# Kernel tuning notes

Hardware: AMD Instinct MI355X
Metric: run time of the kernel (lower is better)

The kernel has to match this reference:

```python
import jax, jax.numpy as jnp
import numpy as np

B, C, H, W = 32, 256, 64, 64
CI = C // 2  # inter_channels


def conv1x1(x, w, b):
    # x: [B, Cin, H, W], w: [Cout, Cin], b: [Cout]
    return jnp.einsum('bchw,oc->bohw', x, w) + b[None, :, None, None]


def setup_inputs() -> dict:
    key = jax.random.key(0)
    ks = jax.random.split(key, 9)
    s_in = 1.0 / np.sqrt(C)
    s_ci = 1.0 / np.sqrt(CI)
    return {
        'x': jax.random.normal(ks[0], (B, C, H, W), dtype=jnp.float32),
        'theta_w': jax.random.normal(ks[1], (CI, C), dtype=jnp.float32) * s_in,
        'theta_b': jax.random.normal(ks[2], (CI,), dtype=jnp.float32) * s_in,
        'phi_w': jax.random.normal(ks[3], (CI, C), dtype=jnp.float32) * s_in,
        'phi_b': jax.random.normal(ks[4], (CI,), dtype=jnp.float32) * s_in,
        'g_w': jax.random.normal(ks[5], (CI, C), dtype=jnp.float32) * s_in,
        'g_b': jax.random.normal(ks[6], (CI,), dtype=jnp.float32) * s_in,
        'out_w': jax.random.normal(ks[7], (C, CI), dtype=jnp.float32) * s_ci,
        'out_b': jax.random.normal(ks[8], (C,), dtype=jnp.float32) * s_ci,
    }


def reference(x, theta_w, theta_b, phi_w, phi_b, g_w, g_b, out_w, out_b):
    b, c, h, w = x.shape
    n = h * w
    theta = conv1x1(x, theta_w, theta_b).reshape(b, CI, n)  # [B, Ci, N]
    phi = conv1x1(x, phi_w, phi_b).reshape(b, CI, n)        # [B, Ci, N]
    g = conv1x1(x, g_w, g_b).reshape(b, CI, n)              # [B, Ci, N]
    # f[b,i,j] = sum_n theta[b,i,n] * phi[b,j,n]  -> [B, Ci, Ci]
    f = jnp.einsum('bin,bjn->bij', theta, phi)
    f_div_c = jax.nn.softmax(f, axis=-1)
    # y[b,j,n] = sum_i f_div_c[b,i,j] * g[b,i,n]  (uses f^T, per the torch permute)
    y = jnp.einsum('bij,bin->bjn', f_div_c, g)  # [B, Ci, N]
    # Faithful to torch: permute(0,2,1).contiguous().view(B, Ci, H, W)
    # -> a memory reshape of the [B, N, Ci] layout, NOT a transpose.
    y = jnp.transpose(y, (0, 2, 1)).reshape(b, CI, h, w)
    y = conv1x1(y, out_w, out_b)  # [B, C, H, W]
    return x + y
```

## Files before the change

### kernel.cpp

```cpp
#include <hip/hip_runtime.h>

#define B_ 32
#define C_ 256
#define CI_ 128
#define N_ 4096

typedef unsigned int u32;
typedef unsigned short u16;
typedef __attribute__((ext_vector_type(8))) short s8v;
typedef __attribute__((ext_vector_type(4))) float f4v;

__device__ __forceinline__ u16 f2bs(float f) {
    union { float f; u32 u; } c; c.f = f;
    u32 u = c.u + 0x7FFFu + ((c.u >> 16) & 1u);
    return (u16)(u >> 16);
}
__device__ __forceinline__ float bs2f(u16 s) {
    union { u32 u; float f; } c; c.u = ((u32)s) << 16; return c.f;
}
__device__ __forceinline__ void split2(float x, u16& h, u16& l) {
    h = f2bs(x);
    l = f2bs(x - bs2f(h));
}

#define MFMA16(a, b, c) __builtin_amdgcn_mfma_f32_16x16x32_bf16((a), (b), (c), 0, 0, 0)

__global__ __launch_bounds__(64) void sx_kernel(
    const float* __restrict__ x, float* __restrict__ sx)
{
    const int t = blockIdx.x, b = blockIdx.y, lane = threadIdx.x;
    const float4* row = (const float4*)(x + ((size_t)(b * C_ + t)) * N_);
    float s = 0.f;
    for (int k = lane; k < N_ / 4; k += 64) {
        float4 v = row[k];
        s += v.x + v.y + v.z + v.w;
    }
    #pragma unroll
    for (int off = 32; off > 0; off >>= 1) s += __shfl_down(s, off);
    if (lane == 0) sx[b * C_ + t] = s;
}

__global__ __launch_bounds__(256) void gram_mfma(
    const float* __restrict__ x, float* __restrict__ outp)
{
    const int zb = blockIdx.z;
    const int b = zb >> 3, ks = zb & 7;
    const int i0 = blockIdx.y * 128, j0 = blockIdx.x * 128;
    const int tid = threadIdx.x;
    const int w = tid >> 6, l = tid & 63, lm = l & 15, lq = l >> 4;

    __shared__ u16 Ah[128 * 40], Al[128 * 40], Bh[128 * 40], Bl[128 * 40];

    f4v acc[2][8];
    #pragma unroll
    for (int mi = 0; mi < 2; ++mi)
        #pragma unroll
        for (int ni = 0; ni < 8; ++ni) acc[mi][ni] = (f4v){0.f, 0.f, 0.f, 0.f};

    const int srow = tid >> 3;
    const int sc4  = (tid & 7) * 4;

    const int kbeg = ks * 512, kend = kbeg + 512;
    for (int k0 = kbeg; k0 < kend; k0 += 32) {
        #pragma unroll
        for (int rr = 0; rr < 4; ++rr) {
            int row = rr * 32 + srow;
            float4 va = *(const float4*)(x + (((size_t)(b * C_ + i0 + row)) << 12) + k0 + sc4);
            float4 vb = *(const float4*)(x + (((size_t)(b * C_ + j0 + row)) << 12) + k0 + sc4);
            u16 h0, h1, h2, h3, l0, l1, l2, l3;
            split2(va.x, h0, l0); split2(va.y, h1, l1);
            split2(va.z, h2, l2); split2(va.w, h3, l3);
            *(uint2*)&Ah[row * 40 + sc4] = make_uint2((u32)h0 | ((u32)h1 << 16),
                                                      (u32)h2 | ((u32)h3 << 16));
            *(uint2*)&Al[row * 40 + sc4] = make_uint2((u32)l0 | ((u32)l1 << 16),
                                                      (u32)l2 | ((u32)l3 << 16));
            split2(vb.x, h0, l0); split2(vb.y, h1, l1);
            split2(vb.z, h2, l2); split2(vb.w, h3, l3);
            *(uint2*)&Bh[row * 40 + sc4] = make_uint2((u32)h0 | ((u32)h1 << 16),
                                                      (u32)h2 | ((u32)h3 << 16));
            *(uint2*)&Bl[row * 40 + sc4] = make_uint2((u32)l0 | ((u32)l1 << 16),
                                                      (u32)l2 | ((u32)l3 << 16));
        }
        __syncthreads();

        const int kofs = lq * 8;
        s8v ah[2], al2[2];
        #pragma unroll
        for (int mi = 0; mi < 2; ++mi) {
            int arow = w * 32 + mi * 16 + lm;
            ah[mi]  = *(const s8v*)&Ah[arow * 40 + kofs];
            al2[mi] = *(const s8v*)&Al[arow * 40 + kofs];
        }
        #pragma unroll
        for (int ni = 0; ni < 8; ++ni) {
            int brow = ni * 16 + lm;
            s8v bh = *(const s8v*)&Bh[brow * 40 + kofs];
            s8v bl = *(const s8v*)&Bl[brow * 40 + kofs];
            #pragma unroll
            for (int mi = 0; mi < 2; ++mi) {
                acc[mi][ni] = MFMA16(ah[mi],  bh, acc[mi][ni]);
                acc[mi][ni] = MFMA16(ah[mi],  bl, acc[mi][ni]);
                acc[mi][ni] = MFMA16(al2[mi], bh, acc[mi][ni]);
            }
        }
        __syncthreads();
    }
    float* Gp = outp + (((size_t)(b * 256 + 128)) << 12) + (size_t)ks * 65536;
    #pragma unroll
    for (int mi = 0; mi < 2; ++mi)
        #pragma unroll
        for (int ni = 0; ni < 8; ++ni)
            #pragma unroll
            for (int r = 0; r < 4; ++r) {
                int gi = i0 + w * 32 + mi * 16 + lq * 4 + r;
                int gj = j0 + ni * 16 + lm;
                Gp[(size_t)gi * 256 + gj] = acc[mi][ni][r];
            }
}

__global__ __launch_bounds__(256) void g_reduce(
    const float* __restrict__ outp, float* __restrict__ G)
{
    int f = blockIdx.x * 256 + threadIdx.x;
    int b = f >> 14;
    int r4 = (f & 16383) << 2;
    const float* src = outp + (((size_t)(b * 256 + 128)) << 12) + r4;
    float4 s = *(const float4*)(src);
    #pragma unroll
    for (int k = 1; k < 8; ++k) {
        float4 v = *(const float4*)(src + (size_t)k * 65536);
        s.x += v.x; s.y += v.y; s.z += v.z; s.w += v.w;
    }
    *(float4*)(G + ((size_t)b << 16) + r4) = s;
}

__global__ __launch_bounds__(512, 2) void mid_kernel(
    const float* __restrict__ G,
    const float* __restrict__ tw, const float* __restrict__ tb,
    const float* __restrict__ pw, const float* __restrict__ pb,
    const float* __restrict__ sx,
    const float* __restrict__ gw, const float* __restrict__ gb,
    u16* __restrict__ Mh, float* __restrict__ rj)
{
    const int b = blockIdx.x;
    const int tid = threadIdx.x;
    const int w = tid >> 6, l = tid & 63, lm = l & 15, lq = l >> 4;
    const int wr = w >> 2, wc = w & 3;

    __shared__ __attribute__((aligned(16))) char smem[157696];
    float* t12s = (float*)(smem + 155648);
    float* sxs  = (float*)(smem + 156672);
    u16* TwTh = (u16*)(smem);
    u16* TwTl = (u16*)(smem + 10240);
    u16* GTh  = (u16*)(smem + 20480);
    u16* GTl  = (u16*)(smem + 40960);
    u16* A1h = (u16*)(smem);
    u16* A1l = (u16*)(smem + 67584);
    u16* PwTh = (u16*)(smem + 135168);
    u16* PwTl = (u16*)(smem + 145408);
    float* Ff = (float*)(smem);
    u16* fsmTh = (u16*)(smem + 69632);
    u16* fsmTl = (u16*)(smem + 104448);
    u16* GwTh = (u16*)(smem);
    u16* GwTl = (u16*)(smem + 20480);

    if (tid < 256) sxs[tid] = sx[b * 256 + tid];
    __syncthreads();
    {
        const int oid = tid >> 1, half = tid & 1;
        const float* wrow = (oid < 128) ? (tw + oid * 256) : (pw + (oid - 128) * 256);
        float s = 0.f;
        for (int t = half * 128; t < half * 128 + 128; ++t) s += wrow[t] * sxs[t];
        s += __shfl_xor(s, 1);
        if (half == 0) t12s[oid] = s;
    }
    __syncthreads();

    f4v acc[4][4];
    #pragma unroll
    for (int mi = 0; mi < 4; ++mi)
        #pragma unroll
        for (int ni = 0; ni < 4; ++ni) acc[mi][ni] = (f4v){0.f, 0.f, 0.f, 0.f};

    for (int t0 = 0; t0 < C_; t0 += 32) {
        {
            int i = tid >> 2, tg = (tid & 3) * 8;
            float4 v0 = *(const float4*)(tw + i * 256 + t0 + tg);
            float4 v1 = *(const float4*)(tw + i * 256 + t0 + tg + 4);
            u16 h0,h1,h2,h3,l0,l1,l2,l3;
            split2(v0.x,h0,l0); split2(v0.y,h1,l1); split2(v0.z,h2,l2); split2(v0.w,h3,l3);
            *(uint2*)&TwTh[i*40+tg]   = make_uint2((u32)h0|((u32)h1<<16),(u32)h2|((u32)h3<<16));
            *(uint2*)&TwTl[i*40+tg]   = make_uint2((u32)l0|((u32)l1<<16),(u32)l2|((u32)l3<<16));
            split2(v1.x,h0,l0); split2(v1.y,h1,l1); split2(v1.z,h2,l2); split2(v1.w,h3,l3);
            *(uint2*)&TwTh[i*40+tg+4] = make_uint2((u32)h0|((u32)h1<<16),(u32)h2|((u32)h3<<16));
            *(uint2*)&TwTl[i*40+tg+4] = make_uint2((u32)l0|((u32)l1<<16),(u32)l2|((u32)l3<<16));
        }
        {
            int u = tid >> 1, tg = (tid & 1) * 16;
            const float* gp = G + ((size_t)b << 16) + (size_t)u * 256 + t0 + tg;
            #pragma unroll
            for (int q = 0; q < 4; ++q) {
                float4 v = *(const float4*)(gp + q * 4);
                u16 h0,h1,h2,h3,l0,l1,l2,l3;
                split2(v.x,h0,l0); split2(v.y,h1,l1); split2(v.z,h2,l2); split2(v.w,h3,l3);
                *(uint2*)&GTh[u*40+tg+q*4] = make_uint2((u32)h0|((u32)h1<<16),(u32)h2|((u32)h3<<16));
                *(uint2*)&GTl[u*40+tg+q*4] = make_uint2((u32)l0|((u32)l1<<16),(u32)l2|((u32)l3<<16));
            }
        }
        __syncthreads();
        const int kofs = lq * 8;
        s8v ah[4], al[4];
        #pragma unroll
        for (int mi = 0; mi < 4; ++mi) {
            int ai = wr * 64 + mi * 16 + lm;
            ah[mi] = *(const s8v*)&TwTh[ai * 40 + kofs];
            al[mi] = *(const s8v*)&TwTl[ai * 40 + kofs];
        }
        #pragma unroll
        for (int ni = 0; ni < 4; ++ni) {
            int bu = wc * 64 + ni * 16 + lm;
            s8v bh = *(const s8v*)&GTh[bu * 40 + kofs];
            s8v bl = *(const s8v*)&GTl[bu * 40 + kofs];
            #pragma unroll
            for (int mi = 0; mi < 4; ++mi) {
                acc[mi][ni] = MFMA16(ah[mi], bh, acc[mi][ni]);
                acc[mi][ni] = MFMA16(ah[mi], bl, acc[mi][ni]);
                acc[mi][ni] = MFMA16(al[mi], bh, acc[mi][ni]);
            }
        }
        __syncthreads();
    }
    #pragma unroll
    for (int mi = 0; mi < 4; ++mi)
        #pragma unroll
        for (int ni = 0; ni < 4; ++ni)
            #pragma unroll
            for (int r = 0; r < 4; ++r) {
                int i = wr * 64 + mi * 16 + lq * 4 + r;
                int u = wc * 64 + ni * 16 + lm;
                u16 h, lo; split2(acc[mi][ni][r], h, lo);
                A1h[i * 264 + u] = h; A1l[i * 264 + u] = lo;
            }
    __syncthreads();

    f4v acc2[4][2];
    #pragma unroll
    for (int mi = 0; mi < 4; ++mi)
        #pragma unroll
        for (int ni = 0; ni < 2; ++ni) acc2[mi][ni] = (f4v){0.f, 0.f, 0.f, 0.f};

    for (int u0 = 0; u0 < C_; u0 += 32) {
        {
            int j = tid >> 2, ug = (tid & 3) * 8;
            float4 v0 = *(const float4*)(pw + j * 256 + u0 + ug);
            float4 v1 = *(const float4*)(pw + j * 256 + u0 + ug + 4);
            u16 h0,h1,h2,h3,l0,l1,l2,l3;
            split2(v0.x,h0,l0); split2(v0.y,h1,l1); split2(v0.z,h2,l2); split2(v0.w,h3,l3);
            *(uint2*)&PwTh[j*40+ug]   = make_uint2((u32)h0|((u32)h1<<16),(u32)h2|((u32)h3<<16));
            *(uint2*)&PwTl[j*40+ug]   = make_uint2((u32)l0|((u32)l1<<16),(u32)l2|((u32)l3<<16));
            split2(v1.x,h0,l0); split2(v1.y,h1,l1); split2(v1.z,h2,l2); split2(v1.w,h3,l3);
            *(uint2*)&PwTh[j*40+ug+4] = make_uint2((u32)h0|((u32)h1<<16),(u32)h2|((u32)h3<<16));
            *(uint2*)&PwTl[j*40+ug+4] = make_uint2((u32)l0|((u32)l1<<16),(u32)l2|((u32)l3<<16));
        }
        __syncthreads();
        const int kofs = lq * 8;
        s8v ah[4], al[4];
        #pragma unroll
        for (int mi = 0; mi < 4; ++mi) {
            int ai = wr * 64 + mi * 16 + lm;
            ah[mi] = *(const s8v*)&A1h[ai * 264 + u0 + kofs];
            al[mi] = *(const s8v*)&A1l[ai * 264 + u0 + kofs];
        }
        #pragma unroll
        for (int ni = 0; ni < 2; ++ni) {
            int bj = wc * 32 + ni * 16 + lm;
            s8v bh = *(const s8v*)&PwTh[bj * 40 + kofs];
            s8v bl = *(const s8v*)&PwTl[bj * 40 + kofs];
            #pragma unroll
            for (int mi = 0; mi < 4; ++mi) {
                acc2[mi][ni] = MFMA16(ah[mi], bh, acc2[mi][ni]);
                acc2[mi][ni] = MFMA16(ah[mi], bl, acc2[mi][ni]);
                acc2[mi][ni] = MFMA16(al[mi], bh, acc2[mi][ni]);
            }
        }
        __syncthreads();
    }
    #pragma unroll
    for (int ni = 0; ni < 2; ++ni) {
        int j = wc * 32 + ni * 16 + lm;
        float pbv = pb[j], t2v = t12s[128 + j];
        #pragma unroll
        for (int mi = 0; mi < 4; ++mi)
            #pragma unroll
            for (int r = 0; r < 4; ++r) {
                int i = wr * 64 + mi * 16 + lq * 4 + r;
                float val = acc2[mi][ni][r] + t12s[i] * pbv
                          + tb[i] * (t2v + 4096.0f * pbv);
                Ff[i * 136 + j] = val;
            }
    }
    __syncthreads();

    {
        const int i = tid >> 2, sub = tid & 3;
        float vv[32];
        #pragma unroll
        for (int c = 0; c < 32; ++c) vv[c] = Ff[i * 136 + sub * 32 + c];
        float m = vv[0];
        #pragma unroll
        for (int c = 1; c < 32; ++c) m = fmaxf(m, vv[c]);
        m = fmaxf(m, __shfl_xor(m, 1));
        m = fmaxf(m, __shfl_xor(m, 2));
        float s = 0.f;
        #pragma unroll
        for (int c = 0; c < 32; ++c) { vv[c] = __expf(vv[c] - m); s += vv[c]; }
        s += __shfl_xor(s, 1);
        s += __shfl_xor(s, 2);
        float inv = 1.0f / s;
        #pragma unroll
        for (int c = 0; c < 32; ++c) {
            int j = sub * 32 + c;
            u16 h, lo; split2(vv[c] * inv, h, lo);
            fsmTh[j * 136 + i] = h; fsmTl[j * 136 + i] = lo;
        }
    }
    __syncthreads();

    if (tid < 128) {
        float s = 0.f;
        for (int i = 0; i < 128; ++i)
            s += (bs2f(fsmTh[tid * 136 + i]) + bs2f(fsmTl[tid * 136 + i])) * gb[i];
        rj[b * 128 + tid] = s;
    }

    f4v acc3[4][4];
    #pragma unroll
    for (int mi = 0; mi < 4; ++mi)
        #pragma unroll
        for (int ni = 0; ni < 4; ++ni) acc3[mi][ni] = (f4v){0.f, 0.f, 0.f, 0.f};

    for (int i0 = 0; i0 < CI_; i0 += 32) {
        {
            int ir = tid >> 4, tg = (tid & 15) * 16;
            const float* gp = gw + (size_t)(i0 + ir) * 256 + tg;
            float vv[16];
            *(float4*)&vv[0]  = *(const float4*)(gp + 0);
            *(float4*)&vv[4]  = *(const float4*)(gp + 4);
            *(float4*)&vv[8]  = *(const float4*)(gp + 8);
            *(float4*)&vv[12] = *(const float4*)(gp + 12);
            const int chb = ir >> 3, il = ir & 7;
            #pragma unroll
            for (int jj = 0; jj < 16; ++jj) {
                int t = tg + jj;
                int ch = chb ^ ((t >> 4) & 3);
                u16 h, lo; split2(vv[jj], h, lo);
                GwTh[t * 40 + ch * 8 + il] = h;
                GwTl[t * 40 + ch * 8 + il] = lo;
            }
        }
        __syncthreads();
        s8v ah[4], al[4];
        #pragma unroll
        for (int mi = 0; mi < 4; ++mi) {
            int aj = wr * 64 + mi * 16 + lm;
            ah[mi] = *(const s8v*)&fsmTh[aj * 136 + i0 + lq * 8];
            al[mi] = *(const s8v*)&fsmTl[aj * 136 + i0 + lq * 8];
        }
        #pragma unroll
        for (int ni = 0; ni < 4; ++ni) {
            int bt = wc * 64 + ni * 16 + lm;
            int co = (lq ^ ((bt >> 4) & 3)) << 3;
            s8v bh = *(const s8v*)&GwTh[bt * 40 + co];
            s8v bl = *(const s8v*)&GwTl[bt * 40 + co];
            #pragma unroll
            for (int mi = 0; mi < 4; ++mi) {
                acc3[mi][ni] = MFMA16(ah[mi], bh, acc3[mi][ni]);
                acc3[mi][ni] = MFMA16(ah[mi], bl, acc3[mi][ni]);
                acc3[mi][ni] = MFMA16(al[mi], bh, acc3[mi][ni]);
            }
        }
        __syncthreads();
    }
    #pragma unroll
    for (int mi = 0; mi < 4; ++mi)
        #pragma unroll
        for (int ni = 0; ni < 4; ++ni)
            #pragma unroll
            for (int r = 0; r < 4; ++r) {
                int j = wr * 64 + mi * 16 + lq * 4 + r;
                int t = wc * 64 + ni * 16 + lm;
                Mh[(size_t)b * 32768 + (size_t)j * 256 + t] = f2bs(acc3[mi][ni][r]);
            }
}

__global__ __launch_bounds__(256) void owh_kernel(
    const float* __restrict__ ow, u16* __restrict__ Owh)
{
    int i = (blockIdx.x * 256 + threadIdx.x) * 4;
    float4 v = *(const float4*)(ow + i);
    u16 a = f2bs(v.x), b = f2bs(v.y), c = f2bs(v.z), d = f2bs(v.w);
    *(uint2*)&Owh[i] = make_uint2((u32)a | ((u32)b << 16), (u32)c | ((u32)d << 16));
}

__global__ __launch_bounds__(256) void y_kernel(
    const u16* __restrict__ Mh, const float* __restrict__ rj,
    const float* __restrict__ x, float* __restrict__ outp)
{
    const int nb = blockIdx.x, b = blockIdx.y;
    const int n0 = nb * 128;
    const int tid = threadIdx.x;
    const int w = tid >> 6, l = tid & 63, lm = l & 15, lq = l >> 4;

    __shared__ u16 Bs[128 * 40];

    f4v acc[2][8];
    #pragma unroll
    for (int mi = 0; mi < 2; ++mi)
        #pragma unroll
        for (int ni = 0; ni < 8; ++ni) acc[mi][ni] = (f4v){0.f, 0.f, 0.f, 0.f};

    const int tt = tid >> 3;
    const int nn0 = (tid & 7) * 16;

    for (int t0 = 0; t0 < C_; t0 += 32) {
        const float* xr = x + (((size_t)(b * C_ + t0 + tt)) << 12) + n0 + nn0;
        float vv[16];
        *(float4*)&vv[0]  = *(const float4*)(xr + 0);
        *(float4*)&vv[4]  = *(const float4*)(xr + 4);
        *(float4*)&vv[8]  = *(const float4*)(xr + 8);
        *(float4*)&vv[12] = *(const float4*)(xr + 12);
        const int chb = tt >> 3, tl = tt & 7;
        #pragma unroll
        for (int j = 0; j < 16; ++j) {
            int row = nn0 + j;
            int ch = chb ^ ((row >> 4) & 3);
            Bs[row * 40 + ch * 8 + tl] = f2bs(vv[j]);
        }
        __syncthreads();

        s8v af[2];
        #pragma unroll
        for (int mi = 0; mi < 2; ++mi)
            af[mi] = *(const s8v*)(Mh + (size_t)b * 32768
                     + (size_t)(w * 32 + mi * 16 + lm) * 256 + t0 + lq * 8);
        #pragma unroll
        for (int ni = 0; ni < 8; ++ni) {
            int row = ni * 16 + lm;
            s8v bf = *(const s8v*)&Bs[row * 40 + ((lq ^ ((row >> 4) & 3)) << 3)];
            acc[0][ni] = MFMA16(af[0], bf, acc[0][ni]);
            acc[1][ni] = MFMA16(af[1], bf, acc[1][ni]);
        }
        __syncthreads();
    }
    #pragma unroll
    for (int mi = 0; mi < 2; ++mi) {
        const int s0 = w * 32 + mi * 16 + lq * 4;
        float rjv[4];
        #pragma unroll
        for (int r = 0; r < 4; ++r) rjv[r] = rj[b * 128 + s0 + r];
        #pragma unroll
        for (int ni = 0; ni < 8; ++ni) {
            int nn = ni * 16 + lm;
            int z = (n0 + nn) >> 5;
            int q = nn & 31;
            float4 st;
            st.x = acc[mi][ni][0] + rjv[0];
            st.y = acc[mi][ni][1] + rjv[1];
            st.z = acc[mi][ni][2] + rjv[2];
            st.w = acc[mi][ni][3] + rjv[3];
            *(float4*)(outp + (((size_t)(b * C_ + z)) << 12) + 128 * q + s0) = st;
        }
    }
}

__global__ __launch_bounds__(256) void out_kernel(
    float* outp, const u16* __restrict__ Owh, const float* __restrict__ ob,
    const float* __restrict__ x)
{
    const int pt = blockIdx.x, b = blockIdx.y;
    const int p0 = pt * 64;
    const int tid = threadIdx.x;
    const int w = tid >> 6, l = tid & 63, lm = l & 15, lq = l >> 4;

    __shared__ __attribute__((aligned(16))) u16 Zs[64 * 136];
    float* Fsc = (float*)Zs;

    const int zz = tid >> 2;
    const int pp0 = (tid & 3) * 16;
    #pragma unroll
    for (int zb = 0; zb < 128; zb += 64) {
        const int zc = zb + zz;
        const float* yr = outp + (((size_t)(b * C_ + zc)) << 12) + p0 + pp0;
        float vv[16];
        *(float4*)&vv[0]  = *(const float4*)(yr + 0);
        *(float4*)&vv[4]  = *(const float4*)(yr + 4);
        *(float4*)&vv[8]  = *(const float4*)(yr + 8);
        *(float4*)&vv[12] = *(const float4*)(yr + 12);
        const int chb = zc >> 3, zl = zc & 7;
        #pragma unroll
        for (int j = 0; j < 16; ++j) {
            int row = pp0 + j;
            int ch = chb ^ ((row >> 4) & 3);
            Zs[row * 136 + ch * 8 + zl] = f2bs(vv[j]);
        }
    }
    __syncthreads();

    f4v acc[4][4];
    #pragma unroll
    for (int mi = 0; mi < 4; ++mi)
        #pragma unroll
        for (int ni = 0; ni < 4; ++ni) acc[mi][ni] = (f4v){0.f, 0.f, 0.f, 0.f};

    #pragma unroll
    for (int kc = 0; kc < 4; ++kc) {
        s8v af[4];
        #pragma unroll
        for (int mi = 0; mi < 4; ++mi)
            af[mi] = *(const s8v*)(Owh + (size_t)(w * 64 + mi * 16 + lm) * 128
                                   + kc * 32 + lq * 8);
        #pragma unroll
        for (int ni = 0; ni < 4; ++ni) {
            int row = ni * 16 + lm;
            s8v bf = *(const s8v*)&Zs[row * 136 + kc * 32
                                      + ((lq ^ ((row >> 4) & 3)) << 3)];
            #pragma unroll
            for (int mi = 0; mi < 4; ++mi)
                acc[mi][ni] = MFMA16(af[mi], bf, acc[mi][ni]);
        }
    }

    #pragma unroll
    for (int mi = 0; mi < 4; ++mi) {
        __syncthreads();
        #pragma unroll
        for (int ni = 0; ni < 4; ++ni)
            #pragma unroll
            for (int r = 0; r < 4; ++r)
                Fsc[(w * 16 + lq * 4 + r) * 68 + ni * 16 + lm] = acc[mi][ni][r];
        __syncthreads();
        #pragma unroll
        for (int k = 0; k < 4; ++k) {
            int g = tid + 256 * k;
            int row = g >> 4, c4 = (g & 15) * 4;
            float4 v = *(const float4*)&Fsc[row * 68 + c4];
            int o = (row >> 4) * 64 + mi * 16 + (row & 15);
            size_t idx = (((size_t)(b * C_ + o)) << 12) + p0 + c4;
            float4 xv = *(const float4*)(x + idx);
            float bo = ob[o];
            float4 st;
            st.x = v.x + bo + xv.x;
            st.y = v.y + bo + xv.y;
            st.z = v.z + bo + xv.z;
            st.w = v.w + bo + xv.w;
            *(float4*)(outp + idx) = st;
        }
    }
}

extern "C" void kernel_launch(void* const* d_in, const int* in_sizes, int n_in,
                              void* d_out, int out_size, void* d_ws, size_t ws_size,
                              hipStream_t stream) {
    const float* x  = (const float*)d_in[0];
    const float* tw = (const float*)d_in[1];
    const float* tb = (const float*)d_in[2];
    const float* pw = (const float*)d_in[3];
    const float* pb = (const float*)d_in[4];
    const float* gw = (const float*)d_in[5];
    const float* gb = (const float*)d_in[6];
    const float* ow = (const float*)d_in[7];
    const float* ob = (const float*)d_in[8];
    float* out = (float*)d_out;

    char* ws = (char*)d_ws;
    float* G   = (float*)(ws);
    float* sx  = (float*)(ws + 8388608ull);
    float* rj  = (float*)(ws + 14712832ull);
    u16*   Mh  = (u16*)(ws + 14729216ull);
    u16*   Owh = (u16*)(ws + 16826368ull);

    hipLaunchKernelGGL(sx_kernel, dim3(C_, B_), dim3(64), 0, stream, x, sx);
    hipLaunchKernelGGL(gram_mfma, dim3(2, 2, B_ * 8), dim3(256), 0, stream, x, out);
    hipLaunchKernelGGL(g_reduce, dim3(2048), dim3(256), 0, stream, out, G);
    hipLaunchKernelGGL(mid_kernel, dim3(B_), dim3(512), 0, stream,
                       G, tw, tb, pw, pb, sx, gw, gb, Mh, rj);
    hipLaunchKernelGGL(owh_kernel, dim3(32), dim3(256), 0, stream, ow, Owh);
    hipLaunchKernelGGL(y_kernel, dim3(32, B_), dim3(256), 0, stream, Mh, rj, x, out);
    hipLaunchKernelGGL(out_kernel, dim3(64, B_), dim3(256), 0, stream, out, Owh, ob, x);
}
```

Before: 482.1 us.

## Exploit Gram symmetry to skip a tile and store intermediate Y as bf16

The Gram kernel now launches 3 tiles per batch split instead of 4, computing only the upper-triangular blocks. Diagonal blocks load the A operand once and reuse it as B. The reduction recovers the missing lower block by reading the transposed upper block. Separately, the y stage writes its intermediate output as bf16 instead of fp32, and out_kernel reads those bf16 values directly, which halves that round trip through memory. The transposed reads in the reduction are strided and uncoalesced, which could cost some of the saving.

```diff
diff --git a/kernel.cpp b/kernel.cpp
--- a/kernel.cpp
+++ b/kernel.cpp
@@ -43,13 +43,17 @@
 __global__ __launch_bounds__(256) void gram_mfma(
     const float* __restrict__ x, float* __restrict__ outp)
 {
-    const int zb = blockIdx.z;
+    const int q = blockIdx.x;
+    const int zb = blockIdx.y;
     const int b = zb >> 3, ks = zb & 7;
-    const int i0 = blockIdx.y * 128, j0 = blockIdx.x * 128;
+    const int i0 = (q == 1) ? 128 : 0;
+    const int j0 = (q == 0) ? 0 : 128;
+    const bool diag = (q < 2);
     const int tid = threadIdx.x;
     const int w = tid >> 6, l = tid & 63, lm = l & 15, lq = l >> 4;
 
-    __shared__ u16 Ah[128 * 40], Al[128 * 40], Bh[128 * 40], Bl[128 * 40];
+    __shared__ u16 S[4 * 5120];
+    const int bb = diag ? 0 : 10240;
 
     f4v acc[2][8];
     #pragma unroll
@@ -66,20 +70,22 @@
         for (int rr = 0; rr < 4; ++rr) {
             int row = rr * 32 + srow;
             float4 va = *(const float4*)(x + (((size_t)(b * C_ + i0 + row)) << 12) + k0 + sc4);
-            float4 vb = *(const float4*)(x + (((size_t)(b * C_ + j0 + row)) << 12) + k0 + sc4);
             u16 h0, h1, h2, h3, l0, l1, l2, l3;
             split2(va.x, h0, l0); split2(va.y, h1, l1);
             split2(va.z, h2, l2); split2(va.w, h3, l3);
-            *(uint2*)&Ah[row * 40 + sc4] = make_uint2((u32)h0 | ((u32)h1 << 16),
-                                                      (u32)h2 | ((u32)h3 << 16));
-            *(uint2*)&Al[row * 40 + sc4] = make_uint2((u32)l0 | ((u32)l1 << 16),
-                                                      (u32)l2 | ((u32)l3 << 16));
-            split2(vb.x, h0, l0); split2(vb.y, h1, l1);
-            split2(vb.z, h2, l2); split2(vb.w, h3, l3);
-            *(uint2*)&Bh[row * 40 + sc4] = make_uint2((u32)h0 | ((u32)h1 << 16),
-                                                      (u32)h2 | ((u32)h3 << 16));
-            *(uint2*)&Bl[row * 40 + sc4] = make_uint2((u32)l0 | ((u32)l1 << 16),
-                                                      (u32)l2 | ((u32)l3 << 16));
+            *(uint2*)&S[row * 40 + sc4]        = make_uint2((u32)h0 | ((u32)h1 << 16),
+                                                            (u32)h2 | ((u32)h3 << 16));
+            *(uint2*)&S[5120 + row * 40 + sc4] = make_uint2((u32)l0 | ((u32)l1 << 16),
+                                                            (u32)l2 | ((u32)l3 << 16));
+            if (!diag) {
+                float4 vb = *(const float4*)(x + (((size_t)(b * C_ + j0 + row)) << 12) + k0 + sc4);
+                split2(vb.x, h0, l0); split2(vb.y, h1, l1);
+                split2(vb.z, h2, l2); split2(vb.w, h3, l3);
+                *(uint2*)&S[10240 + row * 40 + sc4] = make_uint2((u32)h0 | ((u32)h1 << 16),
+                                                                 (u32)h2 | ((u32)h3 << 16));
+                *(uint2*)&S[15360 + row * 40 + sc4] = make_uint2((u32)l0 | ((u32)l1 << 16),
+                                                                 (u32)l2 | ((u32)l3 << 16));
+            }
         }
         __syncthreads();
 
@@ -88,14 +94,14 @@
         #pragma unroll
         for (int mi = 0; mi < 2; ++mi) {
             int arow = w * 32 + mi * 16 + lm;
-            ah[mi]  = *(const s8v*)&Ah[arow * 40 + kofs];
-            al2[mi] = *(const s8v*)&Al[arow * 40 + kofs];
+            ah[mi]  = *(const s8v*)&S[arow * 40 + kofs];
+            al2[mi] = *(const s8v*)&S[5120 + arow * 40 + kofs];
         }
         #pragma unroll
         for (int ni = 0; ni < 8; ++ni) {
             int brow = ni * 16 + lm;
-            s8v bh = *(const s8v*)&Bh[brow * 40 + kofs];
-            s8v bl = *(const s8v*)&Bl[brow * 40 + kofs];
+            s8v bh = *(const s8v*)&S[bb + brow * 40 + kofs];
+            s8v bl = *(const s8v*)&S[bb + 5120 + brow * 40 + kofs];
             #pragma unroll
             for (int mi = 0; mi < 2; ++mi) {
                 acc[mi][ni] = MFMA16(ah[mi],  bh, acc[mi][ni]);
@@ -124,12 +130,28 @@
     int f = blockIdx.x * 256 + threadIdx.x;
     int b = f >> 14;
     int r4 = (f & 16383) << 2;
-    const float* src = outp + (((size_t)(b * 256 + 128)) << 12) + r4;
-    float4 s = *(const float4*)(src);
-    #pragma unroll
-    for (int k = 1; k < 8; ++k) {
-        float4 v = *(const float4*)(src + (size_t)k * 65536);
-        s.x += v.x; s.y += v.y; s.z += v.z; s.w += v.w;
+    int gi = r4 >> 8, gj0 = r4 & 255;
+    const float* base = outp + (((size_t)(b * 256 + 128)) << 12);
+    float4 s;
+    if (gi < 128 || gj0 >= 128) {
+        const float* src = base + r4;
+        s = *(const float4*)(src);
+        #pragma unroll
+        for (int k = 1; k < 8; ++k) {
+            float4 v = *(const float4*)(src + (size_t)k * 65536);
+            s.x += v.x; s.y += v.y; s.z += v.z; s.w += v.w;
+        }
+    } else {
+        float a0 = 0.f, a1 = 0.f, a2 = 0.f, a3 = 0.f;
+        #pragma unroll
+        for (int k = 0; k < 8; ++k) {
+            const float* sp = base + (size_t)k * 65536 + gi;
+            a0 += sp[(size_t)(gj0 + 0) * 256];
+            a1 += sp[(size_t)(gj0 + 1) * 256];
+            a2 += sp[(size_t)(gj0 + 2) * 256];
+            a3 += sp[(size_t)(gj0 + 3) * 256];
+        }
+        s.x = a0; s.y = a1; s.z = a2; s.w = a3;
     }
     *(float4*)(G + ((size_t)b << 16) + r4) = s;
 }
@@ -199,12 +221,12 @@
             int u = tid >> 1, tg = (tid & 1) * 16;
             const float* gp = G + ((size_t)b << 16) + (size_t)u * 256 + t0 + tg;
             #pragma unroll
-            for (int q = 0; q < 4; ++q) {
-                float4 v = *(const float4*)(gp + q * 4);
+            for (int qq = 0; qq < 4; ++qq) {
+                float4 v = *(const float4*)(gp + qq * 4);
                 u16 h0,h1,h2,h3,l0,l1,l2,l3;
                 split2(v.x,h0,l0); split2(v.y,h1,l1); split2(v.z,h2,l2); split2(v.w,h3,l3);
-                *(uint2*)&GTh[u*40+tg+q*4] = make_uint2((u32)h0|((u32)h1<<16),(u32)h2|((u32)h3<<16));
-                *(uint2*)&GTl[u*40+tg+q*4] = make_uint2((u32)l0|((u32)l1<<16),(u32)l2|((u32)l3<<16));
+                *(uint2*)&GTh[u*40+tg+qq*4] = make_uint2((u32)h0|((u32)h1<<16),(u32)h2|((u32)h3<<16));
+                *(uint2*)&GTl[u*40+tg+qq*4] = make_uint2((u32)l0|((u32)l1<<16),(u32)l2|((u32)l3<<16));
             }
         }
         __syncthreads();
@@ -452,6 +474,7 @@
         }
         __syncthreads();
     }
+    u16* Yh = (u16*)(outp + (((size_t)(b * C_)) << 12));
     #pragma unroll
     for (int mi = 0; mi < 2; ++mi) {
         const int s0 = w * 32 + mi * 16 + lq * 4;
@@ -462,13 +485,13 @@
         for (int ni = 0; ni < 8; ++ni) {
             int nn = ni * 16 + lm;
             int z = (n0 + nn) >> 5;
-            int q = nn & 31;
-            float4 st;
-            st.x = acc[mi][ni][0] + rjv[0];
-            st.y = acc[mi][ni][1] + rjv[1];
-            st.z = acc[mi][ni][2] + rjv[2];
-            st.w = acc[mi][ni][3] + rjv[3];
-            *(float4*)(outp + (((size_t)(b * C_ + z)) << 12) + 128 * q + s0) = st;
+            int qq = nn & 31;
+            u16 h0 = f2bs(acc[mi][ni][0] + rjv[0]);
+            u16 h1 = f2bs(acc[mi][ni][1] + rjv[1]);
+            u16 h2 = f2bs(acc[mi][ni][2] + rjv[2]);
+            u16 h3 = f2bs(acc[mi][ni][3] + rjv[3]);
+            *(uint2*)&Yh[(size_t)z * 4096 + 128 * qq + s0] =
+                make_uint2((u32)h0 | ((u32)h1 << 16), (u32)h2 | ((u32)h3 << 16));
         }
     }
 }
@@ -485,23 +508,21 @@
     __shared__ __attribute__((aligned(16))) u16 Zs[64 * 136];
     float* Fsc = (float*)Zs;
 
+    const u16* Yh = (const u16*)(outp + (((size_t)(b * C_)) << 12));
     const int zz = tid >> 2;
     const int pp0 = (tid & 3) * 16;
     #pragma unroll
     for (int zb = 0; zb < 128; zb += 64) {
         const int zc = zb + zz;
-        const float* yr = outp + (((size_t)(b * C_ + zc)) << 12) + p0 + pp0;
-        float vv[16];
-        *(float4*)&vv[0]  = *(const float4*)(yr + 0);
-        *(float4*)&vv[4]  = *(const float4*)(yr + 4);
-        *(float4*)&vv[8]  = *(const float4*)(yr + 8);
-        *(float4*)&vv[12] = *(const float4*)(yr + 12);
+        u16 vv[16];
+        *(uint4*)&vv[0] = *(const uint4*)&Yh[(size_t)zc * 4096 + p0 + pp0];
+        *(uint4*)&vv[8] = *(const uint4*)&Yh[(size_t)zc * 4096 + p0 + pp0 + 8];
         const int chb = zc >> 3, zl = zc & 7;
         #pragma unroll
         for (int j = 0; j < 16; ++j) {
             int row = pp0 + j;
             int ch = chb ^ ((row >> 4) & 3);
-            Zs[row * 136 + ch * 8 + zl] = f2bs(vv[j]);
+            Zs[row * 136 + ch * 8 + zl] = vv[j];
         }
     }
     __syncthreads();
@@ -580,7 +601,7 @@
     u16*   Owh = (u16*)(ws + 16826368ull);
 
     hipLaunchKernelGGL(sx_kernel, dim3(C_, B_), dim3(64), 0, stream, x, sx);
-    hipLaunchKernelGGL(gram_mfma, dim3(2, 2, B_ * 8), dim3(256), 0, stream, x, out);
+    hipLaunchKernelGGL(gram_mfma, dim3(3, B_ * 8), dim3(256), 0, stream, x, out);
     hipLaunchKernelGGL(g_reduce, dim3(2048), dim3(256), 0, stream, out, G);
     hipLaunchKernelGGL(mid_kernel, dim3(B_), dim3(512), 0, stream,
                        G, tw, tb, pw, pb, sx, gw, gb, Mh, rj);
```

Result: slower. 492.4 us (+2.1%).
